# Kernel tuning notes

Measured on AMD Instinct MI355X. Metric: run time of the kernel, lower is better.

The kernel has to match this reference:

```python
import jax, jax.numpy as jnp
import numpy as np

N, E = 50000, 1600000
FEAT, HID, HEADS = 256, 64, 2
NEG_SLOPE = 0.2


def gat_conv(x, src, dst, W, att_src, att_dst, bias, heads, out_ch):
    """PyG GATConv (concat=True, self-loops already appended to src/dst)."""
    n = x.shape[0]
    h = (x @ W).reshape(n, heads, out_ch)                      # [N,H,C]
    a_src = jnp.einsum('nhc,hc->nh', h, att_src)               # [N,H]
    a_dst = jnp.einsum('nhc,hc->nh', h, att_dst)               # [N,H]
    alpha = jax.nn.leaky_relu(a_src[src] + a_dst[dst], NEG_SLOPE)  # [E',H]
    # segment softmax over incoming edges of each dst node
    amax = jax.ops.segment_max(alpha, dst, num_segments=n)
    alpha = jnp.exp(alpha - amax[dst])
    denom = jax.ops.segment_sum(alpha, dst, num_segments=n)
    alpha = alpha / (denom[dst] + 1e-16)
    msg = h[src] * alpha[..., None]                            # [E',H,C]
    out = jax.ops.segment_sum(msg, dst, num_segments=n)        # [N,H,C]
    return out.reshape(n, heads * out_ch) + bias


def setup_inputs() -> dict:
    key = jax.random.key(0)
    ks = jax.random.split(key, 10)
    x = jax.random.normal(ks[0], (N, FEAT), dtype=jnp.float32)
    edge_index = jax.random.randint(ks[1], (2, E), 0, N, dtype=jnp.int64)
    s1 = 1.0 / np.sqrt(FEAT)
    s2 = 1.0 / np.sqrt(HID * HEADS)
    sa = 1.0 / np.sqrt(HID)
    return {
        'x': x,
        'edge_index': edge_index,
        'W1': jax.random.uniform(ks[2], (FEAT, HEADS * HID), jnp.float32, -s1, s1),
        'att_src1': jax.random.uniform(ks[3], (HEADS, HID), jnp.float32, -sa, sa),
        'att_dst1': jax.random.uniform(ks[4], (HEADS, HID), jnp.float32, -sa, sa),
        'b1': jnp.zeros((HEADS * HID,), jnp.float32),
        'W2': jax.random.uniform(ks[5], (HEADS * HID, HID), jnp.float32, -s2, s2),
        'att_src2': jax.random.uniform(ks[6], (1, HID), jnp.float32, -sa, sa),
        'att_dst2': jax.random.uniform(ks[7], (1, HID), jnp.float32, -sa, sa),
        'b2': jnp.zeros((HID,), jnp.float32),
    }


def reference(x, edge_index, W1, att_src1, att_dst1, b1, W2, att_src2, att_dst2, b2):
    n = x.shape[0]
    loop = jnp.arange(n, dtype=edge_index.dtype)
    src = jnp.concatenate([edge_index[0], loop])   # add self loops (PyG default)
    dst = jnp.concatenate([edge_index[1], loop])
    h = gat_conv(x, src, dst, W1, att_src1, att_dst1, b1, HEADS, HID)
    h = jax.nn.relu(h)  # dropout is identity in eval mode
    h = gat_conv(h, src, dst, W2, att_src2, att_dst2, b2, 1, HID)
    return jax.nn.log_softmax(h, axis=1)
```

## Files before the change

### kernel.cpp

```cpp
#include <hip/hip_runtime.h>
#include <hip/hip_bf16.h>
#include <math.h>

typedef short bf16x8 __attribute__((ext_vector_type(8)));
typedef float f32x4 __attribute__((ext_vector_type(4)));

#define BSHIFT 7
#define BWIDTH 128
#define PCHUNK 4096

__global__ void prep_kernel(int* __restrict__ bcnt,
                            const float* __restrict__ W1, const float* __restrict__ W2,
                            __hip_bfloat16* __restrict__ W1t,
                            __hip_bfloat16* __restrict__ W2t) {
    if (blockIdx.x == 0) {
        bcnt[threadIdx.x] = 0;
        bcnt[threadIdx.x + 256] = 0;
        return;
    }
    int idx = (blockIdx.x - 1) * 256 + threadIdx.x;
    const int n1 = 128 * 256;
    if (idx < n1) {
        int nn = idx >> 8, kk = idx & 255;
        W1t[idx] = __float2bfloat16(W1[kk * 128 + nn]);
    } else {
        int j = idx - n1;
        if (j < 64 * 128) {
            int nn = j >> 7, kk = j & 127;
            W2t[j] = __float2bfloat16(W2[kk * 64 + nn]);
        }
    }
}

__global__ __launch_bounds__(256) void bucket_hist(const int* __restrict__ ei, int E,
                                                   int* __restrict__ bcnt) {
    __shared__ int h[512];
    int tid = threadIdx.x;
    for (int i = tid; i < 512; i += 256) h[i] = 0;
    __syncthreads();
    int start = blockIdx.x * PCHUNK;
    int cnt = min(PCHUNK, E - start);
    for (int i = tid; i < cnt; i += 256)
        atomicAdd(&h[ei[E + start + i] >> BSHIFT], 1);
    __syncthreads();
    for (int i = tid; i < 512; i += 256)
        if (h[i]) atomicAdd(&bcnt[i], h[i]);
}

__global__ __launch_bounds__(512) void bucket_scan(const int* __restrict__ bcnt,
                                                   int* __restrict__ bbase,
                                                   int* __restrict__ bcur,
                                                   int nbk, int n) {
    __shared__ int s[512];
    int tid = threadIdx.x;
    int nodes = 0;
    if (tid < nbk) nodes = min(BWIDTH, n - (tid << BSHIFT));
    int v = (tid < nbk) ? bcnt[tid] + nodes : 0;
    s[tid] = v;
    __syncthreads();
    #pragma unroll
    for (int o = 1; o < 512; o <<= 1) {
        int t = (tid >= o) ? s[tid - o] : 0;
        __syncthreads();
        s[tid] += t;
        __syncthreads();
    }
    if (tid < nbk) {
        int ex = s[tid] - v;
        bbase[tid] = ex;
        bcur[tid] = ex - (tid << BSHIFT);
    }
    if (tid == nbk) bbase[nbk] = s[tid];
}

__global__ __launch_bounds__(256) void partition_edges(const int* __restrict__ ei, int E,
                                                       int* __restrict__ bcur,
                                                       int* __restrict__ tmp) {
    __shared__ int2 stage[PCHUNK];
    __shared__ int h[512];
    __shared__ int lbase[512];
    int tid = threadIdx.x;
    int start = blockIdx.x * PCHUNK;
    int cnt = min(PCHUNK, E - start);
    for (int i = tid; i < 512; i += 256) h[i] = 0;
    __syncthreads();
    for (int i = tid; i < cnt; i += 256) {
        int s = ei[start + i];
        int d = ei[E + start + i];
        stage[i] = make_int2(s, d);
        atomicAdd(&h[d >> BSHIFT], 1);
    }
    __syncthreads();
    for (int i = tid; i < 512; i += 256) {
        if (h[i] > 0) lbase[i] = atomicAdd(&bcur[i], h[i]);
        h[i] = 0;
    }
    __syncthreads();
    for (int i = tid; i < cnt; i += 256) {
        int2 e = stage[i];
        int b = e.y >> BSHIFT;
        int r = atomicAdd(&h[b], 1);
        tmp[lbase[b] + r] = (e.x << BSHIFT) | (e.y & (BWIDTH - 1));
    }
}

__global__ __launch_bounds__(256) void bucket_csr(const int* __restrict__ bbase,
                                                  const int* __restrict__ tmp,
                                                  int* __restrict__ offs,
                                                  int* __restrict__ srcs,
                                                  int n, int nbk) {
    __shared__ int cnt[BWIDTH];
    __shared__ int sa[BWIDTH];
    __shared__ int cur[BWIDTH];
    int b = blockIdx.x;
    int tid = threadIdx.x;
    int node0 = b << BSHIFT;
    int nnodes = min(BWIDTH, n - node0);
    int cb = bbase[b];
    int ce = bbase[b + 1];
    int tb = cb - node0;
    int ecnt = (ce - cb) - nnodes;

    if (tid < BWIDTH) cnt[tid] = (tid < nnodes) ? 1 : 0;
    __syncthreads();
    for (int i = tid; i < ecnt; i += 256)
        atomicAdd(&cnt[tmp[tb + i] & (BWIDTH - 1)], 1);
    __syncthreads();
    if (tid < BWIDTH) sa[tid] = cnt[tid];
    __syncthreads();
    #pragma unroll
    for (int o = 1; o < BWIDTH; o <<= 1) {
        int v = 0;
        if (tid < BWIDTH) { v = sa[tid]; if (tid >= o) v += sa[tid - o]; }
        __syncthreads();
        if (tid < BWIDTH) sa[tid] = v;
        __syncthreads();
    }
    if (tid < BWIDTH) {
        int ex = sa[tid] - cnt[tid];
        if (tid < nnodes) {
            offs[node0 + tid] = cb + ex;
            srcs[cb + ex] = node0 + tid;
        }
        cur[tid] = ex + (tid < nnodes ? 1 : 0);
    }
    if (b == nbk - 1 && tid == 0) offs[n] = ce;
    __syncthreads();
    for (int i = tid; i < ecnt; i += 256) {
        int e = tmp[tb + i];
        int li = e & (BWIDTH - 1);
        int r = atomicAdd(&cur[li], 1);
        srcs[cb + r] = e >> BSHIFT;
    }
}

template <bool A_BF16, int NT, int HEADS, int KSTEPS>
__global__ __launch_bounds__(256) void gemm_att(
    const void* __restrict__ Av, const __hip_bfloat16* __restrict__ Bt,
    __hip_bfloat16* __restrict__ C,
    const float* __restrict__ atts, const float* __restrict__ attd,
    float* __restrict__ a_s, float* __restrict__ a_d, int M) {
    constexpr int K = KSTEPS * 32;
    constexpr int N = NT * 16;
    int tid = threadIdx.x;
    int w = tid >> 6, l = tid & 63;
    int q = l >> 4, m16 = l & 15;
    int bm = blockIdx.x * 64;
    int arow = bm + w * 16 + m16;
    if (arow >= M) arow = M - 1;

    f32x4 acc[NT];
    #pragma unroll
    for (int t = 0; t < NT; t++) acc[t] = (f32x4){0.f, 0.f, 0.f, 0.f};

    if (A_BF16) {
        const __hip_bfloat16* A = (const __hip_bfloat16*)Av + (size_t)arow * K + q * 8;
        bf16x8 af[KSTEPS];
        #pragma unroll
        for (int t = 0; t < KSTEPS; t++)
            af[t] = *(const bf16x8*)(A + t * 32);
        #pragma unroll
        for (int t = 0; t < KSTEPS; t++) {
            #pragma unroll
            for (int c = 0; c < NT; c++) {
                bf16x8 b = *(const bf16x8*)(Bt + (size_t)(c * 16 + m16) * K + t * 32 + q * 8);
                acc[c] = __builtin_amdgcn_mfma_f32_16x16x32_bf16(af[t], b, acc[c], 0, 0, 0);
            }
        }
    } else {
        const float* A = (const float*)Av + (size_t)arow * K + q * 8;
        #pragma unroll
        for (int hf = 0; hf < KSTEPS / 4; hf++) {
            float4 st[8];
            #pragma unroll
            for (int t = 0; t < 4; t++) {
                st[2 * t]     = *(const float4*)(A + (hf * 4 + t) * 32);
                st[2 * t + 1] = *(const float4*)(A + (hf * 4 + t) * 32 + 4);
            }
            #pragma unroll
            for (int t = 0; t < 4; t++) {
                union { __hip_bfloat16 h[8]; bf16x8 v; } af;
                float4 v0 = st[2 * t], v1 = st[2 * t + 1];
                af.h[0] = __float2bfloat16(v0.x); af.h[1] = __float2bfloat16(v0.y);
                af.h[2] = __float2bfloat16(v0.z); af.h[3] = __float2bfloat16(v0.w);
                af.h[4] = __float2bfloat16(v1.x); af.h[5] = __float2bfloat16(v1.y);
                af.h[6] = __float2bfloat16(v1.z); af.h[7] = __float2bfloat16(v1.w);
                #pragma unroll
                for (int c = 0; c < NT; c++) {
                    bf16x8 b = *(const bf16x8*)(Bt + (size_t)(c * 16 + m16) * K +
                                                (hf * 4 + t) * 32 + q * 8);
                    acc[c] = __builtin_amdgcn_mfma_f32_16x16x32_bf16(af.v, b, acc[c], 0, 0, 0);
                }
            }
        }
    }

    #pragma unroll
    for (int t = 0; t < NT; t++) {
        #pragma unroll
        for (int r = 0; r < 4; r++) {
            int row = bm + w * 16 + q * 4 + r;
            if (row < M) C[(size_t)row * N + t * 16 + m16] = __float2bfloat16(acc[t][r]);
        }
    }

    float ps[HEADS][4], pd[HEADS][4];
    #pragma unroll
    for (int hh = 0; hh < HEADS; hh++)
        #pragma unroll
        for (int r = 0; r < 4; r++) { ps[hh][r] = 0.f; pd[hh][r] = 0.f; }
    #pragma unroll
    for (int t = 0; t < NT; t++) {
        int ch = t * 16 + m16;
        float asw = atts[ch], adw = attd[ch];
        int hh = (HEADS == 2) ? (t >> 2) : 0;
        #pragma unroll
        for (int r = 0; r < 4; r++) {
            ps[hh][r] = fmaf(acc[t][r], asw, ps[hh][r]);
            pd[hh][r] = fmaf(acc[t][r], adw, pd[hh][r]);
        }
    }
    #pragma unroll
    for (int o = 1; o < 16; o <<= 1) {
        #pragma unroll
        for (int hh = 0; hh < HEADS; hh++)
            #pragma unroll
            for (int r = 0; r < 4; r++) {
                ps[hh][r] += __shfl_xor(ps[hh][r], o);
                pd[hh][r] += __shfl_xor(pd[hh][r], o);
            }
    }
    if (m16 == 0) {
        #pragma unroll
        for (int r = 0; r < 4; r++) {
            int row = bm + w * 16 + q * 4 + r;
            if (row < M) {
                if (HEADS == 2) {
                    a_s[row * 2]     = ps[0][r];
                    a_s[row * 2 + 1] = ps[1][r];
                    a_d[row * 2]     = pd[0][r];
                    a_d[row * 2 + 1] = pd[1][r];
                } else {
                    a_s[row] = ps[0][r];
                    a_d[row] = pd[0][r];
                }
            }
        }
    }
}

__device__ __forceinline__ float leaky(float r) {
    return r < 0.f ? 0.2f * r : r;
}

__device__ __forceinline__ void unpack2(unsigned u, float& lo, float& hi) {
    lo = __uint_as_float(u << 16);
    hi = __uint_as_float(u & 0xffff0000u);
}

__global__ __launch_bounds__(256) void edge_agg_l1(
    const int* __restrict__ offs, const int* __restrict__ srcs,
    const __hip_bfloat16* __restrict__ h1, const float* __restrict__ asv,
    const float* __restrict__ adv, const float* __restrict__ bias,
    __hip_bfloat16* __restrict__ out, int n) {
    int d = (blockIdx.x * blockDim.x + threadIdx.x) >> 6;
    int lane = threadIdx.x & 63;
    if (d >= n) return;
    int start = offs[d], end = offs[d + 1];
    float ad0 = adv[2 * d], ad1 = adv[2 * d + 1];

    int sub = lane & 15;
    int g = lane >> 4;
    int ch0 = sub * 8;
    int hsel = sub >> 3;

    float s0 = 0.f, s1 = 0.f;
    float acc[8];
    #pragma unroll
    for (int k = 0; k < 8; k++) acc[k] = 0.f;

    for (int base = start; base < end; base += 64) {
        int cnt = min(64, end - base);
        int s_l = 0;
        float e0 = 0.f, e1 = 0.f;
        if (lane < cnt) {
            s_l = srcs[base + lane];
            float2 a = *(const float2*)(asv + 2 * s_l);
            e0 = __expf(leaky(a.x + ad0));
            e1 = __expf(leaky(a.y + ad1));
        }
        s0 += e0;
        s1 += e1;

        int steps = (cnt + 3) >> 2;
        int jj = 0;
        for (; jj + 4 <= steps; jj += 4) {
            float wgt[4]; int sr[4];
            #pragma unroll
            for (int u = 0; u < 4; u++) {
                int e = (jj + u) * 4 + g;
                float w0 = __shfl(e0, e);
                float w1 = __shfl(e1, e);
                sr[u] = __shfl(s_l, e);
                wgt[u] = hsel ? w1 : w0;
            }
            uint4 v[4];
            #pragma unroll
            for (int u = 0; u < 4; u++)
                v[u] = *(const uint4*)(h1 + (size_t)sr[u] * 128 + ch0);
            #pragma unroll
            for (int u = 0; u < 4; u++) {
                float f0, f1, f2, f3, f4, f5, f6, f7;
                unpack2(v[u].x, f0, f1); unpack2(v[u].y, f2, f3);
                unpack2(v[u].z, f4, f5); unpack2(v[u].w, f6, f7);
                float wA = wgt[u];
                acc[0] = fmaf(wA, f0, acc[0]); acc[1] = fmaf(wA, f1, acc[1]);
                acc[2] = fmaf(wA, f2, acc[2]); acc[3] = fmaf(wA, f3, acc[3]);
                acc[4] = fmaf(wA, f4, acc[4]); acc[5] = fmaf(wA, f5, acc[5]);
                acc[6] = fmaf(wA, f6, acc[6]); acc[7] = fmaf(wA, f7, acc[7]);
            }
        }
        for (; jj + 2 <= steps; jj += 2) {
            int eA = jj * 4 + g, eB = eA + 4;
            float w0A = __shfl(e0, eA), w1A = __shfl(e1, eA);
            int sA = __shfl(s_l, eA);
            float w0B = __shfl(e0, eB), w1B = __shfl(e1, eB);
            int sB = __shfl(s_l, eB);
            float wA = hsel ? w1A : w0A;
            float wB = hsel ? w1B : w0B;
            uint4 vA = *(const uint4*)(h1 + (size_t)sA * 128 + ch0);
            uint4 vB = *(const uint4*)(h1 + (size_t)sB * 128 + ch0);
            float f0, f1, f2, f3, f4, f5, f6, f7;
            unpack2(vA.x, f0, f1); unpack2(vA.y, f2, f3);
            unpack2(vA.z, f4, f5); unpack2(vA.w, f6, f7);
            acc[0] = fmaf(wA, f0, acc[0]); acc[1] = fmaf(wA, f1, acc[1]);
            acc[2] = fmaf(wA, f2, acc[2]); acc[3] = fmaf(wA, f3, acc[3]);
            acc[4] = fmaf(wA, f4, acc[4]); acc[5] = fmaf(wA, f5, acc[5]);
            acc[6] = fmaf(wA, f6, acc[6]); acc[7] = fmaf(wA, f7, acc[7]);
            unpack2(vB.x, f0, f1); unpack2(vB.y, f2, f3);
            unpack2(vB.z, f4, f5); unpack2(vB.w, f6, f7);
            acc[0] = fmaf(wB, f0, acc[0]); acc[1] = fmaf(wB, f1, acc[1]);
            acc[2] = fmaf(wB, f2, acc[2]); acc[3] = fmaf(wB, f3, acc[3]);
            acc[4] = fmaf(wB, f4, acc[4]); acc[5] = fmaf(wB, f5, acc[5]);
            acc[6] = fmaf(wB, f6, acc[6]); acc[7] = fmaf(wB, f7, acc[7]);
        }
        if (jj < steps) {
            int eA = jj * 4 + g;
            float w0A = __shfl(e0, eA), w1A = __shfl(e1, eA);
            int sA = __shfl(s_l, eA);
            float wA = hsel ? w1A : w0A;
            uint4 vA = *(const uint4*)(h1 + (size_t)sA * 128 + ch0);
            float f0, f1, f2, f3, f4, f5, f6, f7;
            unpack2(vA.x, f0, f1); unpack2(vA.y, f2, f3);
            unpack2(vA.z, f4, f5); unpack2(vA.w, f6, f7);
            acc[0] = fmaf(wA, f0, acc[0]); acc[1] = fmaf(wA, f1, acc[1]);
            acc[2] = fmaf(wA, f2, acc[2]); acc[3] = fmaf(wA, f3, acc[3]);
            acc[4] = fmaf(wA, f4, acc[4]); acc[5] = fmaf(wA, f5, acc[5]);
            acc[6] = fmaf(wA, f6, acc[6]); acc[7] = fmaf(wA, f7, acc[7]);
        }
    }
    #pragma unroll
    for (int o = 16; o < 64; o <<= 1)
        #pragma unroll
        for (int k = 0; k < 8; k++) acc[k] += __shfl_xor(acc[k], o);
    #pragma unroll
    for (int o = 1; o < 64; o <<= 1) {
        s0 += __shfl_xor(s0, o);
        s1 += __shfl_xor(s1, o);
    }

    if (lane < 16) {
        float invh = 1.f / ((hsel ? s1 : s0) + 1e-16f);
        float4 b0 = *(const float4*)(bias + ch0);
        float4 b1 = *(const float4*)(bias + ch0 + 4);
        union { __hip_bfloat16 h[8]; uint4 u; } o2;
        o2.h[0] = __float2bfloat16(fmaxf(fmaf(acc[0], invh, b0.x), 0.f));
        o2.h[1] = __float2bfloat16(fmaxf(fmaf(acc[1], invh, b0.y), 0.f));
        o2.h[2] = __float2bfloat16(fmaxf(fmaf(acc[2], invh, b0.z), 0.f));
        o2.h[3] = __float2bfloat16(fmaxf(fmaf(acc[3], invh, b0.w), 0.f));
        o2.h[4] = __float2bfloat16(fmaxf(fmaf(acc[4], invh, b1.x), 0.f));
        o2.h[5] = __float2bfloat16(fmaxf(fmaf(acc[5], invh, b1.y), 0.f));
        o2.h[6] = __float2bfloat16(fmaxf(fmaf(acc[6], invh, b1.z), 0.f));
        o2.h[7] = __float2bfloat16(fmaxf(fmaf(acc[7], invh, b1.w), 0.f));
        *(uint4*)(out + (size_t)d * 128 + ch0) = o2.u;
    }
}

__global__ __launch_bounds__(256) void edge_agg_l2(
    const int* __restrict__ offs, const int* __restrict__ srcs,
    const __hip_bfloat16* __restrict__ h2, const float* __restrict__ asv,
    const float* __restrict__ adv, const float* __restrict__ bias,
    float* __restrict__ out, int n) {
    int d = (blockIdx.x * blockDim.x + threadIdx.x) >> 6;
    int lane = threadIdx.x & 63;
    if (d >= n) return;
    int start = offs[d], end = offs[d + 1];
    float ad = adv[d];

    int sub = lane & 7;
    int g = lane >> 3;
    int ch0 = sub * 8;

    float ssum = 0.f;
    float acc[8];
    #pragma unroll
    for (int k = 0; k < 8; k++) acc[k] = 0.f;

    for (int base = start; base < end; base += 64) {
        int cnt = min(64, end - base);
        int s_l = 0;
        float ew = 0.f;
        if (lane < cnt) {
            s_l = srcs[base + lane];
            ew = __expf(leaky(asv[s_l] + ad));
        }
        ssum += ew;

        int steps = (cnt + 7) >> 3;
        int jj = 0;
        for (; jj + 4 <= steps; jj += 4) {
            float wgt[4]; int sr[4];
            #pragma unroll
            for (int u = 0; u < 4; u++) {
                int e = (jj + u) * 8 + g;
                wgt[u] = __shfl(ew, e);
                sr[u] = __shfl(s_l, e);
            }
            uint4 v[4];
            #pragma unroll
            for (int u = 0; u < 4; u++)
                v[u] = *(const uint4*)(h2 + (size_t)sr[u] * 64 + ch0);
            #pragma unroll
            for (int u = 0; u < 4; u++) {
                float f0, f1, f2, f3, f4, f5, f6, f7;
                unpack2(v[u].x, f0, f1); unpack2(v[u].y, f2, f3);
                unpack2(v[u].z, f4, f5); unpack2(v[u].w, f6, f7);
                float wA = wgt[u];
                acc[0] = fmaf(wA, f0, acc[0]); acc[1] = fmaf(wA, f1, acc[1]);
                acc[2] = fmaf(wA, f2, acc[2]); acc[3] = fmaf(wA, f3, acc[3]);
                acc[4] = fmaf(wA, f4, acc[4]); acc[5] = fmaf(wA, f5, acc[5]);
                acc[6] = fmaf(wA, f6, acc[6]); acc[7] = fmaf(wA, f7, acc[7]);
            }
        }
        for (; jj + 2 <= steps; jj += 2) {
            int eA = jj * 8 + g, eB = eA + 8;
            float wA = __shfl(ew, eA);
            int sA = __shfl(s_l, eA);
            float wB = __shfl(ew, eB);
            int sB = __shfl(s_l, eB);
            uint4 vA = *(const uint4*)(h2 + (size_t)sA * 64 + ch0);
            uint4 vB = *(const uint4*)(h2 + (size_t)sB * 64 + ch0);
            float f0, f1, f2, f3, f4, f5, f6, f7;
            unpack2(vA.x, f0, f1); unpack2(vA.y, f2, f3);
            unpack2(vA.z, f4, f5); unpack2(vA.w, f6, f7);
            acc[0] = fmaf(wA, f0, acc[0]); acc[1] = fmaf(wA, f1, acc[1]);
            acc[2] = fmaf(wA, f2, acc[2]); acc[3] = fmaf(wA, f3, acc[3]);
            acc[4] = fmaf(wA, f4, acc[4]); acc[5] = fmaf(wA, f5, acc[5]);
            acc[6] = fmaf(wA, f6, acc[6]); acc[7] = fmaf(wA, f7, acc[7]);
            unpack2(vB.x, f0, f1); unpack2(vB.y, f2, f3);
            unpack2(vB.z, f4, f5); unpack2(vB.w, f6, f7);
            acc[0] = fmaf(wB, f0, acc[0]); acc[1] = fmaf(wB, f1, acc[1]);
            acc[2] = fmaf(wB, f2, acc[2]); acc[3] = fmaf(wB, f3, acc[3]);
            acc[4] = fmaf(wB, f4, acc[4]); acc[5] = fmaf(wB, f5, acc[5]);
            acc[6] = fmaf(wB, f6, acc[6]); acc[7] = fmaf(wB, f7, acc[7]);
        }
        if (jj < steps) {
            int eA = jj * 8 + g;
            float wA = __shfl(ew, eA);
            int sA = __shfl(s_l, eA);
            uint4 vA = *(const uint4*)(h2 + (size_t)sA * 64 + ch0);
            float f0, f1, f2, f3, f4, f5, f6, f7;
            unpack2(vA.x, f0, f1); unpack2(vA.y, f2, f3);
            unpack2(vA.z, f4, f5); unpack2(vA.w, f6, f7);
            acc[0] = fmaf(wA, f0, acc[0]); acc[1] = fmaf(wA, f1, acc[1]);
            acc[2] = fmaf(wA, f2, acc[2]); acc[3] = fmaf(wA, f3, acc[3]);
            acc[4] = fmaf(wA, f4, acc[4]); acc[5] = fmaf(wA, f5, acc[5]);
            acc[6] = fmaf(wA, f6, acc[6]); acc[7] = fmaf(wA, f7, acc[7]);
        }
    }
    #pragma unroll
    for (int o = 8; o < 64; o <<= 1)
        #pragma unroll
        for (int k = 0; k < 8; k++) acc[k] += __shfl_xor(acc[k], o);
    #pragma unroll
    for (int o = 1; o < 64; o <<= 1) ssum += __shfl_xor(ssum, o);

    float inv = 1.f / (ssum + 1e-16f);
    float4 b0 = *(const float4*)(bias + ch0);
    float4 b1 = *(const float4*)(bias + ch0 + 4);
    float v[8];
    v[0] = fmaf(acc[0], inv, b0.x); v[1] = fmaf(acc[1], inv, b0.y);
    v[2] = fmaf(acc[2], inv, b0.z); v[3] = fmaf(acc[3], inv, b0.w);
    v[4] = fmaf(acc[4], inv, b1.x); v[5] = fmaf(acc[5], inv, b1.y);
    v[6] = fmaf(acc[6], inv, b1.z); v[7] = fmaf(acc[7], inv, b1.w);

    float vm = v[0];
    #pragma unroll
    for (int k = 1; k < 8; k++) vm = fmaxf(vm, v[k]);
    #pragma unroll
    for (int o = 1; o < 8; o <<= 1) vm = fmaxf(vm, __shfl_xor(vm, o));
    float se_loc = 0.f;
    #pragma unroll
    for (int k = 0; k < 8; k++) se_loc += __expf(v[k] - vm);
    #pragma unroll
    for (int o = 1; o < 8; o <<= 1) se_loc += __shfl_xor(se_loc, o);
    float lse = vm + logf(se_loc);

    if (lane < 8) {
        float4 o0 = make_float4(v[0] - lse, v[1] - lse, v[2] - lse, v[3] - lse);
        float4 o1 = make_float4(v[4] - lse, v[5] - lse, v[6] - lse, v[7] - lse);
        *(float4*)(out + (size_t)d * 64 + ch0) = o0;
        *(float4*)(out + (size_t)d * 64 + ch0 + 4) = o1;
    }
}

extern "C" void kernel_launch(void* const* d_in, const int* in_sizes, int n_in,
                              void* d_out, int out_size, void* d_ws, size_t ws_size,
                              hipStream_t stream) {
    const float* x    = (const float*)d_in[0];
    const int*   ei   = (const int*)d_in[1];
    const float* W1   = (const float*)d_in[2];
    const float* as1w = (const float*)d_in[3];
    const float* ad1w = (const float*)d_in[4];
    const float* b1   = (const float*)d_in[5];
    const float* W2   = (const float*)d_in[6];
    const float* as2w = (const float*)d_in[7];
    const float* ad2w = (const float*)d_in[8];
    const float* b2   = (const float*)d_in[9];
    float* out = (float*)d_out;

    const int n = in_sizes[0] / 256;
    const int E = in_sizes[1] / 2;
    const int tot = E + n;
    const int nbk = (n + BWIDTH - 1) / BWIDTH;

    char* p = (char*)d_ws;
    auto alloc = [&](size_t bytes) {
        void* r = (void*)p;
        p += (bytes + 255) & ~(size_t)255;
        return r;
    };
    int*   offs  = (int*)alloc((size_t)(n + 1) * 4);
    int*   srcs  = (int*)alloc((size_t)tot * 4);
    int*   tmp   = (int*)alloc((size_t)E * 4);
    int*   bcnt  = (int*)alloc(512 * 4);
    int*   bbase = (int*)alloc(512 * 4);
    int*   bcur  = (int*)alloc(512 * 4);
    __hip_bfloat16* W1t = (__hip_bfloat16*)alloc((size_t)128 * 256 * 2);
    __hip_bfloat16* W2t = (__hip_bfloat16*)alloc((size_t)64 * 128 * 2);
    __hip_bfloat16* h1  = (__hip_bfloat16*)alloc((size_t)n * 128 * 2);
    __hip_bfloat16* out1= (__hip_bfloat16*)alloc((size_t)n * 128 * 2);
    __hip_bfloat16* h2  = (__hip_bfloat16*)alloc((size_t)n * 64 * 2);
    float* a_s1 = (float*)alloc((size_t)n * 2 * 4);
    float* a_d1 = (float*)alloc((size_t)n * 2 * 4);
    float* a_s2 = (float*)alloc((size_t)n * 4);
    float* a_d2 = (float*)alloc((size_t)n * 4);

    int pblocks = (E + PCHUNK - 1) / PCHUNK;

    prep_kernel<<<1 + (128 * 256 + 64 * 128 + 255) / 256, 256, 0, stream>>>(
        bcnt, W1, W2, W1t, W2t);

    bucket_hist<<<pblocks, 256, 0, stream>>>(ei, E, bcnt);
    bucket_scan<<<1, 512, 0, stream>>>(bcnt, bbase, bcur, nbk, n);
    partition_edges<<<pblocks, 256, 0, stream>>>(ei, E, bcur, tmp);
    bucket_csr<<<nbk, 256, 0, stream>>>(bbase, tmp, offs, srcs, n, nbk);

    gemm_att<false, 8, 2, 8><<<(n + 63) / 64, 256, 0, stream>>>(
        x, W1t, h1, as1w, ad1w, a_s1, a_d1, n);
    edge_agg_l1<<<((size_t)n * 64 + 255) / 256, 256, 0, stream>>>(
        offs, srcs, h1, a_s1, a_d1, b1, out1, n);

    gemm_att<true, 4, 1, 4><<<(n + 63) / 64, 256, 0, stream>>>(
        out1, W2t, h2, as2w, ad2w, a_s2, a_d2, n);
    edge_agg_l2<<<((size_t)n * 64 + 255) / 256, 256, 0, stream>>>(
        offs, srcs, h2, a_s2, a_d2, b2, out, n);
}
```

Baseline: 285.6 us.

## Stage GEMM weight tiles in LDS and split layer-1 aggregation launch

The GEMM+attention kernel now copies each 128-wide K chunk of the transposed weight matrix into padded shared memory and reads B fragments from LDS instead of global memory. The fp32 and bf16 A paths are merged into one chunked loop. This adds barriers and LDS use per block, which may lower occupancy. Separately, the layer-1 edge aggregation is split into two launches over halves of the destination nodes. That split adds a launch with no clear benefit, and may be an experiment.

```diff
diff --git a/kernel.cpp b/kernel.cpp
--- a/kernel.cpp
+++ b/kernel.cpp
@@ -162,6 +162,11 @@
     float* __restrict__ a_s, float* __restrict__ a_d, int M) {
     constexpr int K = KSTEPS * 32;
     constexpr int N = NT * 16;
+    constexpr int KH = 128;
+    constexpr int NCH = (K + KH - 1) / KH;
+    constexpr int LDB = KH + 8;
+    __shared__ __hip_bfloat16 Bs[N][LDB];
+
     int tid = threadIdx.x;
     int w = tid >> 6, l = tid & 63;
     int q = l >> 4, m16 = l & 15;
@@ -173,46 +178,51 @@
     #pragma unroll
     for (int t = 0; t < NT; t++) acc[t] = (f32x4){0.f, 0.f, 0.f, 0.f};
 
-    if (A_BF16) {
-        const __hip_bfloat16* A = (const __hip_bfloat16*)Av + (size_t)arow * K + q * 8;
-        bf16x8 af[KSTEPS];
-        #pragma unroll
-        for (int t = 0; t < KSTEPS; t++)
-            af[t] = *(const bf16x8*)(A + t * 32);
-        #pragma unroll
-        for (int t = 0; t < KSTEPS; t++) {
+    #pragma unroll
+    for (int ch = 0; ch < NCH; ch++) {
+        const int cb = ch * KH;
+        bf16x8 af[4];
+        float4 st[8];
+        if (A_BF16) {
+            const __hip_bfloat16* A = (const __hip_bfloat16*)Av + (size_t)arow * K + cb + q * 8;
+            #pragma unroll
+            for (int t = 0; t < 4; t++)
+                af[t] = *(const bf16x8*)(A + t * 32);
+        } else {
+            const float* A = (const float*)Av + (size_t)arow * K + cb + q * 8;
+            #pragma unroll
+            for (int t = 0; t < 4; t++) {
+                st[2 * t]     = *(const float4*)(A + t * 32);
+                st[2 * t + 1] = *(const float4*)(A + t * 32 + 4);
+            }
+        }
+        for (int i = tid; i < (N * KH) / 8; i += 256) {
+            int row = i >> 4;
+            int k = (i & 15) * 8;
+            *(uint4*)&Bs[row][k] = *(const uint4*)(Bt + (size_t)row * K + cb + k);
+        }
+        __syncthreads();
+        if (!A_BF16) {
+            #pragma unroll
+            for (int t = 0; t < 4; t++) {
+                union { __hip_bfloat16 h[8]; bf16x8 v; } u;
+                float4 v0 = st[2 * t], v1 = st[2 * t + 1];
+                u.h[0] = __float2bfloat16(v0.x); u.h[1] = __float2bfloat16(v0.y);
+                u.h[2] = __float2bfloat16(v0.z); u.h[3] = __float2bfloat16(v0.w);
+                u.h[4] = __float2bfloat16(v1.x); u.h[5] = __float2bfloat16(v1.y);
+                u.h[6] = __float2bfloat16(v1.z); u.h[7] = __float2bfloat16(v1.w);
+                af[t] = u.v;
+            }
+        }
+        #pragma unroll
+        for (int t = 0; t < 4; t++) {
             #pragma unroll
             for (int c = 0; c < NT; c++) {
-                bf16x8 b = *(const bf16x8*)(Bt + (size_t)(c * 16 + m16) * K + t * 32 + q * 8);
+                bf16x8 b = *(const bf16x8*)&Bs[c * 16 + m16][t * 32 + q * 8];
                 acc[c] = __builtin_amdgcn_mfma_f32_16x16x32_bf16(af[t], b, acc[c], 0, 0, 0);
             }
         }
-    } else {
-        const float* A = (const float*)Av + (size_t)arow * K + q * 8;
-        #pragma unroll
-        for (int hf = 0; hf < KSTEPS / 4; hf++) {
-            float4 st[8];
-            #pragma unroll
-            for (int t = 0; t < 4; t++) {
-                st[2 * t]     = *(const float4*)(A + (hf * 4 + t) * 32);
-                st[2 * t + 1] = *(const float4*)(A + (hf * 4 + t) * 32 + 4);
-            }
-            #pragma unroll
-            for (int t = 0; t < 4; t++) {
-                union { __hip_bfloat16 h[8]; bf16x8 v; } af;
-                float4 v0 = st[2 * t], v1 = st[2 * t + 1];
-                af.h[0] = __float2bfloat16(v0.x); af.h[1] = __float2bfloat16(v0.y);
-                af.h[2] = __float2bfloat16(v0.z); af.h[3] = __float2bfloat16(v0.w);
-                af.h[4] = __float2bfloat16(v1.x); af.h[5] = __float2bfloat16(v1.y);
-                af.h[6] = __float2bfloat16(v1.z); af.h[7] = __float2bfloat16(v1.w);
-                #pragma unroll
-                for (int c = 0; c < NT; c++) {
-                    bf16x8 b = *(const bf16x8*)(Bt + (size_t)(c * 16 + m16) * K +
-                                                (hf * 4 + t) * 32 + q * 8);
-                    acc[c] = __builtin_amdgcn_mfma_f32_16x16x32_bf16(af.v, b, acc[c], 0, 0, 0);
-                }
-            }
-        }
+        if (ch + 1 < NCH) __syncthreads();
     }
 
     #pragma unroll
@@ -282,10 +292,10 @@
     const int* __restrict__ offs, const int* __restrict__ srcs,
     const __hip_bfloat16* __restrict__ h1, const float* __restrict__ asv,
     const float* __restrict__ adv, const float* __restrict__ bias,
-    __hip_bfloat16* __restrict__ out, int n) {
-    int d = (blockIdx.x * blockDim.x + threadIdx.x) >> 6;
+    __hip_bfloat16* __restrict__ out, int d0, int dlim) {
+    int d = d0 + ((blockIdx.x * blockDim.x + threadIdx.x) >> 6);
     int lane = threadIdx.x & 63;
-    if (d >= n) return;
+    if (d >= dlim) return;
     int start = offs[d], end = offs[d + 1];
     float ad0 = adv[2 * d], ad1 = adv[2 * d + 1];
 
@@ -588,8 +598,11 @@
 
     gemm_att<false, 8, 2, 8><<<(n + 63) / 64, 256, 0, stream>>>(
         x, W1t, h1, as1w, ad1w, a_s1, a_d1, n);
-    edge_agg_l1<<<((size_t)n * 64 + 255) / 256, 256, 0, stream>>>(
-        offs, srcs, h1, a_s1, a_d1, b1, out1, n);
+    int nh = n / 2;
+    edge_agg_l1<<<((size_t)nh * 64 + 255) / 256, 256, 0, stream>>>(
+        offs, srcs, h1, a_s1, a_d1, b1, out1, 0, nh);
+    edge_agg_l1<<<((size_t)(n - nh) * 64 + 255) / 256, 256, 0, stream>>>(
+        offs, srcs, h1, a_s1, a_d1, b1, out1, nh, n);
 
     gemm_att<true, 4, 1, 4><<<(n + 63) / 64, 256, 0, stream>>>(
         out1, W2t, h2, as2w, ad2w, a_s2, a_d2, n);
```

Measured after the change: 268.4 us. 6.0% less time.
